# Kernel optimization log

Measured on AMD Instinct MI355X. Metric: run time of the kernel, lower is better.

Reference implementation:

```python
import jax, jax.numpy as jnp
import numpy as np

DT = 0.05      # bsde.delta_t
EPS = 1e-6     # BatchNormalization epsilon


def _bn(x, gamma, beta):
    # training-mode batch norm: statistics over the batch axis
    m = jnp.mean(x, axis=0, keepdims=True)
    v = jnp.var(x, axis=0, keepdims=True)
    return (x - m) * jax.lax.rsqrt(v + EPS) * gamma + beta


def _subnet(x, g0, b0, W0, g1, b1, W1, g2, b2, W2, bias2, g3, b3):
    # bn -> (dense -> bn -> relu) x 2 -> dense(+bias) -> bn
    x = _bn(x, g0, b0)
    x = jax.nn.relu(_bn(x @ W0, g1, b1))
    x = jax.nn.relu(_bn(x @ W1, g2, b2))
    x = _bn(x @ W2 + bias2, g3, b3)
    return x


def setup_inputs() -> dict:
    key = jax.random.key(0)
    B, D, N, H = 8192, 100, 20, 110
    T = N - 1  # number of subnets
    ks = jax.random.split(key, 18)
    u = lambda k, s, lo, hi: jax.random.uniform(k, s, jnp.float32, lo, hi)
    s_dh = np.sqrt(2.0 / (D + H)).astype(np.float32)
    s_hh = np.sqrt(2.0 / (H + H)).astype(np.float32)
    s_hd = np.sqrt(2.0 / (H + D)).astype(np.float32)
    return {
        "dw": jax.random.normal(ks[0], (B, D, N), jnp.float32) * np.sqrt(DT).astype(np.float32),
        "x": jax.random.normal(ks[1], (B, D, N + 1), jnp.float32),
        "mean_y_input": jax.random.normal(ks[2], (N,), jnp.float32),
        "y_init": u(ks[3], (1,), 0.0, 1.0),
        "z_init": u(ks[4], (1, D), -0.1, 0.1),
        "gamma0": u(ks[5], (T, D), 0.1, 0.5),
        "beta0": 0.1 * jax.random.normal(ks[6], (T, D), jnp.float32),
        "W0": s_dh * jax.random.normal(ks[7], (T, D, H), jnp.float32),
        "gamma1": u(ks[8], (T, H), 0.1, 0.5),
        "beta1": 0.1 * jax.random.normal(ks[9], (T, H), jnp.float32),
        "W1": s_hh * jax.random.normal(ks[10], (T, H, H), jnp.float32),
        "gamma2": u(ks[11], (T, H), 0.1, 0.5),
        "beta2": 0.1 * jax.random.normal(ks[12], (T, H), jnp.float32),
        "W2": s_hd * jax.random.normal(ks[13], (T, H, D), jnp.float32),
        "bias2": jnp.zeros((T, D), jnp.float32),
        "gamma3": u(ks[14], (T, D), 0.1, 0.5),
        "beta3": 0.1 * jax.random.normal(ks[15], (T, D), jnp.float32),
    }


def reference(dw, x, mean_y_input, y_init, z_init, gamma0, beta0, W0,
              gamma1, beta1, W1, gamma2, beta2, W2, bias2, gamma3, beta3):
    B, D, N = dw.shape
    T = N - 1
    # z at step t+1 depends only on x[:, :, t+1] and subnet t -> compute all in parallel
    x_steps = jnp.moveaxis(x[:, :, 1:N], 2, 0)  # [T, B, D]
    z_all = jax.vmap(_subnet)(x_steps, gamma0, beta0, W0, gamma1, beta1, W1,
                              gamma2, beta2, W2, bias2, gamma3, beta3) / D  # [T, B, D]
    z0 = jnp.broadcast_to(z_init, (B, D))          # all_one_vec @ z_init
    zs = jnp.concatenate([z0[None], z_all], axis=0)  # [N, B, D] (z used at each update)
    dw_steps = jnp.moveaxis(dw, 2, 0)               # [N, B, D]
    y0 = jnp.ones((B, 1), dw.dtype) * y_init

    def step(y, zd):
        z, dwt = zd
        # f_tf(t, x, y, z) = sin(y) for the SineBM equation
        y_new = y - DT * jnp.sin(y) + jnp.sum(z * dwt, axis=1, keepdims=True)
        return y_new, jnp.mean(y_new)

    y_final, means = jax.lax.scan(step, y0, (zs, dw_steps))
    mean_y = jnp.concatenate([jnp.mean(y0)[None], means[:T]])  # length N
    return y_final, mean_y
```

## Files before the change

### kernel.cpp

```cpp
#include <hip/hip_runtime.h>

typedef unsigned short u16;
typedef unsigned int   u32;

#define BATCH  8192
#define DIM    100
#define HID    110
#define TSUB   19
#define NSTEP  20
#define KP     128
#define NPAD   112
#define BN_EPS 1e-6f
#define DT_C   0.05f

#define SAB  1024
#define SAR  (BATCH / SAB)
#define SLICES 32

#define A3P  101

typedef __bf16 v8bf __attribute__((ext_vector_type(8)));
typedef float  v4f  __attribute__((ext_vector_type(4)));
typedef float  v2f  __attribute__((ext_vector_type(2)));
typedef u16    u16x4 __attribute__((ext_vector_type(4)));

__device__ __forceinline__ u16 f2bf(float f) {
    u32 u = __float_as_uint(f);
    return (u16)((u + 0x7fffu + ((u >> 16) & 1u)) >> 16);
}
__device__ __forceinline__ float bf2f(u16 h) {
    return __uint_as_float(((u32)h) << 16);
}
__device__ __forceinline__ void acc4(float4& s, float4& q, float4 v) {
    s.x += v.x; s.y += v.y; s.z += v.z; s.w += v.w;
    q.x += v.x * v.x; q.y += v.y * v.y; q.z += v.z * v.z; q.w += v.w * v.w;
}

__global__ void statsA(const float* __restrict__ x, float* __restrict__ part,
                       u32* __restrict__ xT32) {
    __shared__ u16 xls[SAR][2112];
    const int tid = threadIdx.x;
    const int b0 = blockIdx.x * SAR;
    float4 s0 = {0,0,0,0}, q0 = {0,0,0,0};
    float4 s1 = {0,0,0,0}, q1 = {0,0,0,0};
    float4 s2 = {0,0,0,0}, q2 = {0,0,0,0};
#pragma unroll
    for (int r = 0; r < SAR; r++) {
        const float4* row = (const float4*)(x + (size_t)(b0 + r) * 2100);
        float4 v0 = row[tid];
        float4 v1 = row[tid + 256];
        acc4(s0, q0, v0);
        acc4(s1, q1, v1);
        u16x4 p0 = { f2bf(v0.x), f2bf(v0.y), f2bf(v0.z), f2bf(v0.w) };
        u16x4 p1 = { f2bf(v1.x), f2bf(v1.y), f2bf(v1.z), f2bf(v1.w) };
        *(u16x4*)&xls[r][tid * 4]        = p0;
        *(u16x4*)&xls[r][1024 + tid * 4] = p1;
        if (tid < 13) {
            float4 v2 = row[tid + 512];
            acc4(s2, q2, v2);
            u16x4 p2 = { f2bf(v2.x), f2bf(v2.y), f2bf(v2.z), f2bf(v2.w) };
            *(u16x4*)&xls[r][2048 + tid * 4] = p2;
        }
    }
    float* ps = part + (size_t)blockIdx.x * 4200;
    *(float4*)&ps[tid * 4]               = s0;
    *(float4*)&ps[1024 + tid * 4]        = s1;
    *(float4*)&ps[2100 + tid * 4]        = q0;
    *(float4*)&ps[2100 + 1024 + tid * 4] = q1;
    if (tid < 13) {
        *(float4*)&ps[2048 + tid * 4]        = s2;
        *(float4*)&ps[2100 + 2048 + tid * 4] = q2;
    }
    __syncthreads();
    const int TOT = TSUB * SAR * (NPAD / 2);
    for (int i = tid; i < TOT; i += 256) {
        int w = i % (NPAD / 2);
        int seg = i / (NPAD / 2);
        int r = seg % SAR, t = seg / SAR;
        int d0 = w * 2;
        u32 v = 0;
        if (d0 < DIM) {
            u16 lo = xls[r][d0 * 21 + t + 1];
            u16 hi = (d0 + 1 < DIM) ? xls[r][(d0 + 1) * 21 + t + 1] : (u16)0;
            v = (u32)lo | ((u32)hi << 16);
        }
        xT32[((size_t)t * BATCH + b0 + r) * (NPAD / 2) + w] = v;
    }
}

__global__ void statsB(const float* __restrict__ part, float* __restrict__ out) {
    int gid = blockIdx.x * 256 + threadIdx.x;
    if (gid >= 4200 * SLICES) return;
    int slice = gid / 4200;
    int o = gid - slice * 4200;
    const float* p = part + (size_t)slice * (SAB / SLICES) * 4200 + o;
    float acc = 0.f;
#pragma unroll 4
    for (int i = 0; i < SAB / SLICES; i++) acc += p[(size_t)i * 4200];
    atomicAdd(&out[o], acc);
}

__global__ void wtrans(const float* __restrict__ W0, const float* __restrict__ W1,
                       const float* __restrict__ W2, u16* __restrict__ WTsw) {
    __shared__ float lw[HID * HID];
    const int t = blockIdx.x, l = blockIdx.y, tid = threadIdx.x;
    const float* W; int K, N;
    if (l == 0)      { W = W0; K = DIM; N = HID; }
    else if (l == 1) { W = W1; K = HID; N = HID; }
    else             { W = W2; K = HID; N = DIM; }
    const float* Wt = W + (size_t)t * K * N;
    for (int i = tid; i < K * N; i += 256) lw[i] = Wt[i];
    __syncthreads();
    u16* out = WTsw + ((size_t)l * TSUB + t) * (NPAD * KP);
    for (int i = tid; i < NPAD * 16; i += 256) {
        int n = i / 16, p = i % 16;
        int kc = p ^ (n & 7);
        u16 o8[8];
#pragma unroll
        for (int j = 0; j < 8; j++) {
            int k = kc * 8 + j;
            float v = (k < K && n < N) ? lw[k * N + n] : 0.f;
            o8[j] = f2bf(v);
        }
        *(uint4*)&out[(size_t)n * KP + p * 8] = *(uint4*)o8;
    }
}

template <int KREAL, int NOUT, int IDXMODE, int RELU, int BMAJOR>
__global__ void gemm_kernel(const u16* __restrict__ Ain,
                            const u16* __restrict__ WTswL,
                            const float* __restrict__ sumIn,
                            const float* __restrict__ sqIn,
                            const float* __restrict__ gIn,
                            const float* __restrict__ bIn,
                            u16* __restrict__ Hout,
                            float* __restrict__ sumArr,
                            float* __restrict__ sqArr) {
    __shared__ __align__(16) u16 Alds[128 * KP];
    __shared__ __align__(16) u16 Blds[NPAD * KP];
    __shared__ float s_sum[NPAD], s_sq[NPAD];
    __shared__ float aAffL[KP], cAffL[KP];

    const int tid = threadIdx.x;
    const int mt = blockIdx.x;
    const int t  = blockIdx.y;
    const int brow0 = mt * 128;

    if (tid < NPAD) { s_sum[tid] = 0.f; s_sq[tid] = 0.f; }
    if (tid < KREAL) {
        int idx = (IDXMODE == 0) ? (tid * 21 + (t + 1)) : (t * KREAL + tid);
        float m = sumIn[idx] * (1.f / BATCH);
        float v = sqIn[idx] * (1.f / BATCH) - m * m;
        float rstd = rsqrtf(v + BN_EPS);
        float ga = gIn[t * KREAL + tid] * rstd;
        aAffL[tid] = ga;
        cAffL[tid] = bIn[t * KREAL + tid] - m * ga;
    }

    {
        const uint4* wsrc = (const uint4*)(WTswL + (size_t)t * NPAD * KP);
        uint4* bl = (uint4*)Blds;
#pragma unroll
        for (int i = 0; i < 7; i++) bl[tid + i * 256] = wsrc[tid + i * 256];
    }
    const int NCH = (KREAL + 7) / 8;
    for (int i = tid; i < 128 * (16 - NCH); i += 256) {
        int row = i / (16 - NCH);
        int kc  = NCH + i % (16 - NCH);
        uint4 z = {0, 0, 0, 0};
        *(uint4*)&Alds[row * KP + (kc ^ (row & 7)) * 8] = z;
    }
    __syncthreads();

    for (int cidx = tid; cidx < 128 * NCH; cidx += 256) {
        int row = cidx / NCH;
        int kc  = cidx % NCH;
        int k0  = kc * 8;
        const u16* hrow = Ain + ((size_t)t * BATCH + brow0 + row) * NPAD + k0;
        u16 hv[8];
        *(uint4*)hv = *(const uint4*)hrow;
        u16 pk[8];
#pragma unroll
        for (int j = 0; j < 8; j++) {
            int k = k0 + j;
            float av = (k < KREAL) ? fmaf(bf2f(hv[j]), aAffL[k], cAffL[k]) : 0.f;
            if (RELU) av = fmaxf(av, 0.f);
            pk[j] = f2bf(av);
        }
        *(uint4*)&Alds[row * KP + ((kc ^ (row & 7)) * 8)] = *(uint4*)pk;
    }
    __syncthreads();

    const int lane = tid & 63;
    const int wv   = tid >> 6;
    const int r0   = lane & 15;
    const int q    = lane >> 4;
    const int moff = wv * 32;

    v4f acc[2][7];
#pragma unroll
    for (int i = 0; i < 2; i++)
#pragma unroll
        for (int j = 0; j < 7; j++) { v4f z = {0.f, 0.f, 0.f, 0.f}; acc[i][j] = z; }

#pragma unroll
    for (int ks = 0; ks < 4; ks++) {
        int cbase = ks * 4 + q;
        v8bf afr[2];
#pragma unroll
        for (int mf = 0; mf < 2; mf++) {
            int row = moff + mf * 16 + r0;
            afr[mf] = *(const v8bf*)&Alds[row * KP + ((cbase ^ (row & 7)) * 8)];
        }
#pragma unroll
        for (int nf = 0; nf < 7; nf++) {
            int nr = nf * 16 + r0;
            v8bf bfr = *(const v8bf*)&Blds[nr * KP + ((cbase ^ (nr & 7)) * 8)];
            acc[0][nf] = __builtin_amdgcn_mfma_f32_16x16x32_bf16(afr[0], bfr, acc[0][nf], 0, 0, 0);
            acc[1][nf] = __builtin_amdgcn_mfma_f32_16x16x32_bf16(afr[1], bfr, acc[1][nf], 0, 0, 0);
        }
    }

#pragma unroll
    for (int mf = 0; mf < 2; mf++) {
#pragma unroll
        for (int nf = 0; nf < 7; nf++) {
            int n = nf * 16 + r0;
#pragma unroll
            for (int rg = 0; rg < 4; rg++) {
                int grow = brow0 + moff + mf * 16 + q * 4 + rg;
                size_t oidx = BMAJOR ? ((size_t)grow * (TSUB * NPAD) + (size_t)t * NPAD + n)
                                     : (((size_t)t * BATCH + grow) * NPAD + n);
                Hout[oidx] = f2bf(acc[mf][nf][rg]);
            }
        }
    }
#pragma unroll
    for (int nf = 0; nf < 7; nf++) {
        float cs = 0.f, cq = 0.f;
#pragma unroll
        for (int mf = 0; mf < 2; mf++)
#pragma unroll
            for (int rg = 0; rg < 4; rg++) {
                float vv = acc[mf][nf][rg];
                cs += vv; cq += vv * vv;
            }
        cs += __shfl_xor(cs, 16); cs += __shfl_xor(cs, 32);
        cq += __shfl_xor(cq, 16); cq += __shfl_xor(cq, 32);
        if (q == 0) {
            atomicAdd(&s_sum[nf * 16 + r0], cs);
            atomicAdd(&s_sq[nf * 16 + r0], cq);
        }
    }
    __syncthreads();
    if (tid < NOUT) {
        atomicAdd(&sumArr[t * NOUT + tid], s_sum[tid]);
        atomicAdd(&sqArr[t * NOUT + tid], s_sq[tid]);
    }
}

__global__ __launch_bounds__(256, 3)
void scan_kernel(const float* __restrict__ dw,
                 const u16* __restrict__ zbuf,
                 const float* __restrict__ sum3, const float* __restrict__ sq3,
                 const float* __restrict__ g3, const float* __restrict__ b3,
                 const float* __restrict__ z_init, const float* __restrict__ y_init,
                 float* __restrict__ yout, float* __restrict__ meanout) {
    __shared__ float a3l[TSUB * A3P], c3l[TSUB * A3P];
    __shared__ float bsum[NSTEP];
    const int tid = threadIdx.x;
    for (int i = tid; i < TSUB * DIM; i += 256) {
        int t = i / DIM, d = i - t * DIM;
        float m = sum3[i] * (1.f / BATCH);
        float v = sq3[i] * (1.f / BATCH) - m * m;
        float rstd = rsqrtf(v + BN_EPS);
        float ga = g3[i] * rstd;
        a3l[t * A3P + d] = ga * (1.f / DIM);
        c3l[t * A3P + d] = (b3[i] - m * ga) * (1.f / DIM);
    }
    if (tid < NSTEP) bsum[tid] = 0.f;
    __syncthreads();

    const int wv = tid >> 6, lane = tid & 63;
    const int b = blockIdx.x * 4 + wv;
    const int ll = (lane < 50) ? lane : 49;

    v4f w[10];
    u32 zr[TSUB];
    v2f zi;
    {
        const float* dwaddr = dw + (size_t)b * (DIM * NSTEP) + ll * 40;
        const u16*   zaddr  = zbuf + (size_t)b * (TSUB * NPAD) + 2 * ll;
        const float* ziaddr = z_init + 2 * ll;
        asm volatile("global_load_dwordx4 %0, %1, off offset:0"   : "=v"(w[0]) : "v"(dwaddr));
        asm volatile("global_load_dwordx4 %0, %1, off offset:16"  : "=v"(w[1]) : "v"(dwaddr));
        asm volatile("global_load_dwordx4 %0, %1, off offset:32"  : "=v"(w[2]) : "v"(dwaddr));
        asm volatile("global_load_dwordx4 %0, %1, off offset:48"  : "=v"(w[3]) : "v"(dwaddr));
        asm volatile("global_load_dwordx4 %0, %1, off offset:64"  : "=v"(w[4]) : "v"(dwaddr));
        asm volatile("global_load_dwordx4 %0, %1, off offset:80"  : "=v"(w[5]) : "v"(dwaddr));
        asm volatile("global_load_dwordx4 %0, %1, off offset:96"  : "=v"(w[6]) : "v"(dwaddr));
        asm volatile("global_load_dwordx4 %0, %1, off offset:112" : "=v"(w[7]) : "v"(dwaddr));
        asm volatile("global_load_dwordx4 %0, %1, off offset:128" : "=v"(w[8]) : "v"(dwaddr));
        asm volatile("global_load_dwordx4 %0, %1, off offset:144" : "=v"(w[9]) : "v"(dwaddr));
#pragma unroll
        for (int t = 0; t < TSUB; t++)
            asm volatile("global_load_dword %0, %1, off offset:%2"
                         : "=v"(zr[t]) : "v"(zaddr), "i"(t * NPAD * 2));
        asm volatile("global_load_dwordx2 %0, %1, off" : "=v"(zi) : "v"(ziaddr));
        asm volatile("s_waitcnt vmcnt(0)" ::: "memory");
        __builtin_amdgcn_sched_barrier(0);
    }

    float acc[NSTEP];
#pragma unroll
    for (int k = 0; k < NSTEP; k++) acc[k] = 0.f;
    if (lane < 50) {
        const int dbase = 2 * lane;
        acc[0] = zi[0] * w[0][0] + zi[1] * w[5][0];
#pragma unroll
        for (int t = 0; t < TSUB; t++) {
            float a0 = a3l[t * A3P + dbase],     c0 = c3l[t * A3P + dbase];
            float a1 = a3l[t * A3P + dbase + 1], c1 = c3l[t * A3P + dbase + 1];
            u32 z = zr[t];
            float za0 = fmaf(bf2f((u16)(z & 0xffffu)), a0, c0);
            float za1 = fmaf(bf2f((u16)(z >> 16)),     a1, c1);
            const int n = t + 1, j = n >> 2, k = n & 3;
            acc[n] += w[j][k] * za0 + w[5 + j][k] * za1;
        }
    }

#pragma unroll
    for (int m = 1; m < 64; m <<= 1) {
#pragma unroll
        for (int k = 0; k < NSTEP; k++) acc[k] += __shfl_xor(acc[k], m, 64);
    }

    const float yi = y_init[0];
    float y = yi, ysave = 0.f;
#pragma unroll
    for (int i = 0; i < NSTEP; i++) {
        y = y - DT_C * __sinf(y) + acc[i];
        if (i == lane - 1) ysave = y;
    }
    if (lane == 0) yout[b] = y;
    if (lane >= 1 && lane < NSTEP) atomicAdd(&bsum[lane], ysave);
    __syncthreads();
    if (tid >= 1 && tid < NSTEP) atomicAdd(&meanout[tid], bsum[tid] * (1.f / BATCH));
    if (blockIdx.x == 0 && tid == 0) meanout[0] = yi;
}

extern "C" void kernel_launch(void* const* d_in, const int* in_sizes, int n_in,
                              void* d_out, int out_size, void* d_ws, size_t ws_size,
                              hipStream_t stream) {
    const float* dw     = (const float*)d_in[0];
    const float* x      = (const float*)d_in[1];
    const float* y_init = (const float*)d_in[3];
    const float* z_init = (const float*)d_in[4];
    const float* g0 = (const float*)d_in[5];
    const float* b0 = (const float*)d_in[6];
    const float* W0 = (const float*)d_in[7];
    const float* g1 = (const float*)d_in[8];
    const float* b1 = (const float*)d_in[9];
    const float* W1 = (const float*)d_in[10];
    const float* g2 = (const float*)d_in[11];
    const float* b2 = (const float*)d_in[12];
    const float* W2 = (const float*)d_in[13];
    const float* g3 = (const float*)d_in[15];
    const float* b3 = (const float*)d_in[16];

    char* ws = (char*)d_ws;
    size_t off = 0;
    auto alloc = [&](size_t bytes) -> void* {
        off = (off + 255) & ~(size_t)255;
        void* p = ws + off;
        off += bytes;
        return p;
    };

    const int nStats = 4200 + TSUB * HID * 2 * 2 + TSUB * DIM * 2;
    float* statsBlk = (float*)alloc((size_t)nStats * 4);
    float* sum0 = statsBlk;            float* sq0  = sum0 + 2100;
    float* sum1 = sum0 + 4200;         float* sq1  = sum1 + TSUB * HID;
    float* sum2 = sq1 + TSUB * HID;    float* sq2  = sum2 + TSUB * HID;
    float* sum3 = sq2 + TSUB * HID;    float* sq3  = sum3 + TSUB * DIM;

    u16* WTsw = (u16*)alloc((size_t)3 * TSUB * NPAD * KP * 2);

    const size_t hBytes = (size_t)TSUB * BATCH * NPAD * 2;
    u16* h0 = (u16*)alloc(hBytes);
    u16* h1 = (u16*)alloc(hBytes);
    u16* outbuf = h0;
    float* part = (float*)h0;
    u32*  xT32  = (u32*)h1;

    float* yout = (float*)d_out;
    float* meanout = yout + BATCH;

    hipMemsetAsync(statsBlk, 0, (size_t)nStats * 4, stream);
    hipMemsetAsync(meanout, 0, NSTEP * 4, stream);

    wtrans<<<dim3(TSUB, 3), 256, 0, stream>>>(W0, W1, W2, WTsw);
    statsA<<<SAB, 256, 0, stream>>>(x, part, xT32);
    statsB<<<(4200 * SLICES + 255) / 256, 256, 0, stream>>>(part, sum0);

    const u16* xT = (const u16*)xT32;
    u16* WT0 = WTsw;
    u16* WT1 = WTsw + (size_t)TSUB * NPAD * KP;
    u16* WT2 = WTsw + (size_t)2 * TSUB * NPAD * KP;

    gemm_kernel<DIM, HID, 0, 0, 0><<<dim3(64, TSUB), 256, 0, stream>>>(xT, WT0, sum0, sq0, g0, b0, h0, sum1, sq1);
    gemm_kernel<HID, HID, 1, 1, 0><<<dim3(64, TSUB), 256, 0, stream>>>(h0, WT1, sum1, sq1, g1, b1, h1, sum2, sq2);
    gemm_kernel<HID, DIM, 1, 1, 1><<<dim3(64, TSUB), 256, 0, stream>>>(h1, WT2, sum2, sq2, g2, b2, outbuf, sum3, sq3);

    scan_kernel<<<2048, 256, 0, stream>>>(dw, outbuf, sum3, sq3, g3, b3, z_init, y_init, yout, meanout);
}
```

Baseline: 195.6 us.

## Precompute final BN coefficients in separate kernel and stage scan inputs via coalesced LDS loads

Moves the per-block recomputation of the last batch-norm scale and shift (done by all 2048 scan blocks) into a tiny finalize3 kernel that writes packed float4 coefficients once. The scan kernel now loads each block's dw and z rows cooperatively with coalesced float4/u32 loads into swizzled shared memory instead of per-lane strided global loads. This cuts redundant rsqrt work and uncoalesced traffic, but adds an extra kernel launch and a block-wide barrier before compute.

```diff
diff --git a/kernel.cpp b/kernel.cpp
--- a/kernel.cpp
+++ b/kernel.cpp
@@ -17,11 +17,8 @@
 #define SAR  (BATCH / SAB)
 #define SLICES 32
 
-#define A3P  101
-
 typedef __bf16 v8bf __attribute__((ext_vector_type(8)));
 typedef float  v4f  __attribute__((ext_vector_type(4)));
-typedef float  v2f  __attribute__((ext_vector_type(2)));
 typedef u16    u16x4 __attribute__((ext_vector_type(4)));
 
 __device__ __forceinline__ u16 f2bf(float f) {
@@ -259,71 +256,75 @@
     }
 }
 
+__global__ void finalize3(const float* __restrict__ sum3, const float* __restrict__ sq3,
+                          const float* __restrict__ g3, const float* __restrict__ b3,
+                          float4* __restrict__ acg) {
+    int i = blockIdx.x * 256 + threadIdx.x;
+    if (i >= TSUB * 50) return;
+    int t = i / 50, p = i - t * 50;
+    int e = t * DIM + 2 * p;
+    float4 o;
+#pragma unroll
+    for (int h = 0; h < 2; h++) {
+        float m = sum3[e + h] * (1.f / BATCH);
+        float v = sq3[e + h] * (1.f / BATCH) - m * m;
+        float rstd = rsqrtf(v + BN_EPS);
+        float ga = g3[e + h] * rstd * (1.f / DIM);
+        float cc = b3[e + h] * (1.f / DIM) - m * ga;
+        if (h == 0) { o.x = ga; o.y = cc; } else { o.z = ga; o.w = cc; }
+    }
+    acg[i] = o;
+}
+
 __global__ __launch_bounds__(256, 3)
 void scan_kernel(const float* __restrict__ dw,
                  const u16* __restrict__ zbuf,
-                 const float* __restrict__ sum3, const float* __restrict__ sq3,
-                 const float* __restrict__ g3, const float* __restrict__ b3,
+                 const float4* __restrict__ acg,
                  const float* __restrict__ z_init, const float* __restrict__ y_init,
                  float* __restrict__ yout, float* __restrict__ meanout) {
-    __shared__ float a3l[TSUB * A3P], c3l[TSUB * A3P];
+    __shared__ __align__(16) float dwlds[4 * 512 * 4];
+    __shared__ u32 zlds[4 * 1064];
     __shared__ float bsum[NSTEP];
     const int tid = threadIdx.x;
-    for (int i = tid; i < TSUB * DIM; i += 256) {
-        int t = i / DIM, d = i - t * DIM;
-        float m = sum3[i] * (1.f / BATCH);
-        float v = sq3[i] * (1.f / BATCH) - m * m;
-        float rstd = rsqrtf(v + BN_EPS);
-        float ga = g3[i] * rstd;
-        a3l[t * A3P + d] = ga * (1.f / DIM);
-        c3l[t * A3P + d] = (b3[i] - m * ga) * (1.f / DIM);
-    }
+    const int b0 = blockIdx.x * 4;
+
+    const float4* dwg = (const float4*)(dw + (size_t)b0 * (DIM * NSTEP));
+    for (int c = tid; c < 2000; c += 256) {
+        int row = c / 500, cr = c - row * 500;
+        int sw = cr ^ ((cr >> 3) & 7);
+        *(float4*)&dwlds[(row * 512 + sw) * 4] = dwg[c];
+    }
+    const u32* zg = (const u32*)(zbuf + (size_t)b0 * (TSUB * NPAD));
+    for (int u = tid; u < 4 * 1064; u += 256) zlds[u] = zg[u];
     if (tid < NSTEP) bsum[tid] = 0.f;
     __syncthreads();
 
     const int wv = tid >> 6, lane = tid & 63;
-    const int b = blockIdx.x * 4 + wv;
+    const int b = b0 + wv;
     const int ll = (lane < 50) ? lane : 49;
 
     v4f w[10];
-    u32 zr[TSUB];
-    v2f zi;
-    {
-        const float* dwaddr = dw + (size_t)b * (DIM * NSTEP) + ll * 40;
-        const u16*   zaddr  = zbuf + (size_t)b * (TSUB * NPAD) + 2 * ll;
-        const float* ziaddr = z_init + 2 * ll;
-        asm volatile("global_load_dwordx4 %0, %1, off offset:0"   : "=v"(w[0]) : "v"(dwaddr));
-        asm volatile("global_load_dwordx4 %0, %1, off offset:16"  : "=v"(w[1]) : "v"(dwaddr));
-        asm volatile("global_load_dwordx4 %0, %1, off offset:32"  : "=v"(w[2]) : "v"(dwaddr));
-        asm volatile("global_load_dwordx4 %0, %1, off offset:48"  : "=v"(w[3]) : "v"(dwaddr));
-        asm volatile("global_load_dwordx4 %0, %1, off offset:64"  : "=v"(w[4]) : "v"(dwaddr));
-        asm volatile("global_load_dwordx4 %0, %1, off offset:80"  : "=v"(w[5]) : "v"(dwaddr));
-        asm volatile("global_load_dwordx4 %0, %1, off offset:96"  : "=v"(w[6]) : "v"(dwaddr));
-        asm volatile("global_load_dwordx4 %0, %1, off offset:112" : "=v"(w[7]) : "v"(dwaddr));
-        asm volatile("global_load_dwordx4 %0, %1, off offset:128" : "=v"(w[8]) : "v"(dwaddr));
-        asm volatile("global_load_dwordx4 %0, %1, off offset:144" : "=v"(w[9]) : "v"(dwaddr));
-#pragma unroll
-        for (int t = 0; t < TSUB; t++)
-            asm volatile("global_load_dword %0, %1, off offset:%2"
-                         : "=v"(zr[t]) : "v"(zaddr), "i"(t * NPAD * 2));
-        asm volatile("global_load_dwordx2 %0, %1, off" : "=v"(zi) : "v"(ziaddr));
-        asm volatile("s_waitcnt vmcnt(0)" ::: "memory");
-        __builtin_amdgcn_sched_barrier(0);
+    const float* dwbase = &dwlds[wv * 512 * 4];
+#pragma unroll
+    for (int j = 0; j < 10; j++) {
+        int cr = ll * 10 + j;
+        int sw = cr ^ ((cr >> 3) & 7);
+        w[j] = *(const v4f*)&dwbase[sw * 4];
     }
 
     float acc[NSTEP];
 #pragma unroll
     for (int k = 0; k < NSTEP; k++) acc[k] = 0.f;
     if (lane < 50) {
-        const int dbase = 2 * lane;
-        acc[0] = zi[0] * w[0][0] + zi[1] * w[5][0];
+        float2 zi = *(const float2*)(z_init + 2 * ll);
+        acc[0] = zi.x * w[0][0] + zi.y * w[5][0];
+        const u32* zrow = &zlds[wv * 1064];
 #pragma unroll
         for (int t = 0; t < TSUB; t++) {
-            float a0 = a3l[t * A3P + dbase],     c0 = c3l[t * A3P + dbase];
-            float a1 = a3l[t * A3P + dbase + 1], c1 = c3l[t * A3P + dbase + 1];
-            u32 z = zr[t];
-            float za0 = fmaf(bf2f((u16)(z & 0xffffu)), a0, c0);
-            float za1 = fmaf(bf2f((u16)(z >> 16)),     a1, c1);
+            float4 ac = acg[t * 50 + ll];
+            u32 z = zrow[t * 56 + ll];
+            float za0 = fmaf(bf2f((u16)(z & 0xffffu)), ac.x, ac.y);
+            float za1 = fmaf(bf2f((u16)(z >> 16)),     ac.z, ac.w);
             const int n = t + 1, j = n >> 2, k = n & 3;
             acc[n] += w[j][k] * za0 + w[5 + j][k] * za1;
         }
@@ -385,6 +386,7 @@
     float* sum3 = sq2 + TSUB * HID;    float* sq3  = sum3 + TSUB * DIM;
 
     u16* WTsw = (u16*)alloc((size_t)3 * TSUB * NPAD * KP * 2);
+    float4* acg = (float4*)alloc((size_t)TSUB * 50 * 16);
 
     const size_t hBytes = (size_t)TSUB * BATCH * NPAD * 2;
     u16* h0 = (u16*)alloc(hBytes);
@@ -412,5 +414,6 @@
     gemm_kernel<HID, HID, 1, 1, 0><<<dim3(64, TSUB), 256, 0, stream>>>(h0, WT1, sum1, sq1, g1, b1, h1, sum2, sq2);
     gemm_kernel<HID, DIM, 1, 1, 1><<<dim3(64, TSUB), 256, 0, stream>>>(h1, WT2, sum2, sq2, g2, b2, outbuf, sum3, sq3);
 
-    scan_kernel<<<2048, 256, 0, stream>>>(dw, outbuf, sum3, sq3, g3, b3, z_init, y_init, yout, meanout);
-}
+    finalize3<<<4, 256, 0, stream>>>(sum3, sq3, g3, b3, acg);
+    scan_kernel<<<2048, 256, 0, stream>>>(dw, outbuf, acg, z_init, y_init, yout, meanout);
+}
```

New measurement: 202.9 us. +3.7%, slower.

## Widen GEMM blocks to 512 threads, hoist BN3 finalize, replace mean atomics

Applied to the files above, without the earlier changes.

The three GEMM kernels now launch 512 threads per block, with each wave owning 16 rows instead of 32. This halves per-thread accumulators and adds more waves to hide latency, while LDS usage per block stays the same. The BN3 affine coefficients are computed once in a small finalize kernel instead of in every scan block, removing redundant per-block prologue work and 15KB of shared memory. The global atomic mean accumulation is replaced by per-block partials plus a separate reduction kernel, which costs two extra launches.

```diff
diff --git a/kernel.cpp b/kernel.cpp
--- a/kernel.cpp
+++ b/kernel.cpp
@@ -16,8 +16,7 @@
 #define SAB  1024
 #define SAR  (BATCH / SAB)
 #define SLICES 32
-
-#define A3P  101
+#define NBLK_SCAN 2048
 
 typedef __bf16 v8bf __attribute__((ext_vector_type(8)));
 typedef float  v4f  __attribute__((ext_vector_type(4)));
@@ -127,15 +126,16 @@
 }
 
 template <int KREAL, int NOUT, int IDXMODE, int RELU, int BMAJOR>
-__global__ void gemm_kernel(const u16* __restrict__ Ain,
-                            const u16* __restrict__ WTswL,
-                            const float* __restrict__ sumIn,
-                            const float* __restrict__ sqIn,
-                            const float* __restrict__ gIn,
-                            const float* __restrict__ bIn,
-                            u16* __restrict__ Hout,
-                            float* __restrict__ sumArr,
-                            float* __restrict__ sqArr) {
+__global__ __launch_bounds__(512, 2)
+void gemm_kernel(const u16* __restrict__ Ain,
+                 const u16* __restrict__ WTswL,
+                 const float* __restrict__ sumIn,
+                 const float* __restrict__ sqIn,
+                 const float* __restrict__ gIn,
+                 const float* __restrict__ bIn,
+                 u16* __restrict__ Hout,
+                 float* __restrict__ sumArr,
+                 float* __restrict__ sqArr) {
     __shared__ __align__(16) u16 Alds[128 * KP];
     __shared__ __align__(16) u16 Blds[NPAD * KP];
     __shared__ float s_sum[NPAD], s_sq[NPAD];
@@ -160,11 +160,10 @@
     {
         const uint4* wsrc = (const uint4*)(WTswL + (size_t)t * NPAD * KP);
         uint4* bl = (uint4*)Blds;
-#pragma unroll
-        for (int i = 0; i < 7; i++) bl[tid + i * 256] = wsrc[tid + i * 256];
+        for (int i = tid; i < NPAD * KP / 8; i += 512) bl[i] = wsrc[i];
     }
     const int NCH = (KREAL + 7) / 8;
-    for (int i = tid; i < 128 * (16 - NCH); i += 256) {
+    for (int i = tid; i < 128 * (16 - NCH); i += 512) {
         int row = i / (16 - NCH);
         int kc  = NCH + i % (16 - NCH);
         uint4 z = {0, 0, 0, 0};
@@ -172,7 +171,7 @@
     }
     __syncthreads();
 
-    for (int cidx = tid; cidx < 128 * NCH; cidx += 256) {
+    for (int cidx = tid; cidx < 128 * NCH; cidx += 512) {
         int row = cidx / NCH;
         int kc  = cidx % NCH;
         int k0  = kc * 8;
@@ -195,56 +194,44 @@
     const int wv   = tid >> 6;
     const int r0   = lane & 15;
     const int q    = lane >> 4;
-    const int moff = wv * 32;
-
-    v4f acc[2][7];
-#pragma unroll
-    for (int i = 0; i < 2; i++)
-#pragma unroll
-        for (int j = 0; j < 7; j++) { v4f z = {0.f, 0.f, 0.f, 0.f}; acc[i][j] = z; }
+    const int moff = wv * 16;
+
+    v4f acc[7];
+#pragma unroll
+    for (int j = 0; j < 7; j++) { v4f z = {0.f, 0.f, 0.f, 0.f}; acc[j] = z; }
 
 #pragma unroll
     for (int ks = 0; ks < 4; ks++) {
         int cbase = ks * 4 + q;
-        v8bf afr[2];
-#pragma unroll
-        for (int mf = 0; mf < 2; mf++) {
-            int row = moff + mf * 16 + r0;
-            afr[mf] = *(const v8bf*)&Alds[row * KP + ((cbase ^ (row & 7)) * 8)];
-        }
+        int row = moff + r0;
+        v8bf afr = *(const v8bf*)&Alds[row * KP + ((cbase ^ (row & 7)) * 8)];
 #pragma unroll
         for (int nf = 0; nf < 7; nf++) {
             int nr = nf * 16 + r0;
             v8bf bfr = *(const v8bf*)&Blds[nr * KP + ((cbase ^ (nr & 7)) * 8)];
-            acc[0][nf] = __builtin_amdgcn_mfma_f32_16x16x32_bf16(afr[0], bfr, acc[0][nf], 0, 0, 0);
-            acc[1][nf] = __builtin_amdgcn_mfma_f32_16x16x32_bf16(afr[1], bfr, acc[1][nf], 0, 0, 0);
-        }
-    }
-
-#pragma unroll
-    for (int mf = 0; mf < 2; mf++) {
-#pragma unroll
-        for (int nf = 0; nf < 7; nf++) {
-            int n = nf * 16 + r0;
-#pragma unroll
-            for (int rg = 0; rg < 4; rg++) {
-                int grow = brow0 + moff + mf * 16 + q * 4 + rg;
-                size_t oidx = BMAJOR ? ((size_t)grow * (TSUB * NPAD) + (size_t)t * NPAD + n)
-                                     : (((size_t)t * BATCH + grow) * NPAD + n);
-                Hout[oidx] = f2bf(acc[mf][nf][rg]);
-            }
+            acc[nf] = __builtin_amdgcn_mfma_f32_16x16x32_bf16(afr, bfr, acc[nf], 0, 0, 0);
+        }
+    }
+
+#pragma unroll
+    for (int nf = 0; nf < 7; nf++) {
+        int n = nf * 16 + r0;
+#pragma unroll
+        for (int rg = 0; rg < 4; rg++) {
+            int grow = brow0 + moff + q * 4 + rg;
+            size_t oidx = BMAJOR ? ((size_t)grow * (TSUB * NPAD) + (size_t)t * NPAD + n)
+                                 : (((size_t)t * BATCH + grow) * NPAD + n);
+            Hout[oidx] = f2bf(acc[nf][rg]);
         }
     }
 #pragma unroll
     for (int nf = 0; nf < 7; nf++) {
         float cs = 0.f, cq = 0.f;
 #pragma unroll
-        for (int mf = 0; mf < 2; mf++)
-#pragma unroll
-            for (int rg = 0; rg < 4; rg++) {
-                float vv = acc[mf][nf][rg];
-                cs += vv; cq += vv * vv;
-            }
+        for (int rg = 0; rg < 4; rg++) {
+            float vv = acc[nf][rg];
+            cs += vv; cq += vv * vv;
+        }
         cs += __shfl_xor(cs, 16); cs += __shfl_xor(cs, 32);
         cq += __shfl_xor(cq, 16); cq += __shfl_xor(cq, 32);
         if (q == 0) {
@@ -259,25 +246,34 @@
     }
 }
 
+__global__ void finalize3(const float* __restrict__ sum3, const float* __restrict__ sq3,
+                          const float* __restrict__ g3, const float* __restrict__ b3,
+                          float4* __restrict__ acg) {
+    int i = blockIdx.x * 256 + threadIdx.x;
+    if (i >= TSUB * 50) return;
+    int t = i / 50, p = i - t * 50;
+    int e = t * DIM + 2 * p;
+    float4 o;
+#pragma unroll
+    for (int h = 0; h < 2; h++) {
+        float m = sum3[e + h] * (1.f / BATCH);
+        float v = sq3[e + h] * (1.f / BATCH) - m * m;
+        float rstd = rsqrtf(v + BN_EPS);
+        float ga = g3[e + h] * rstd * (1.f / DIM);
+        float cc = b3[e + h] * (1.f / DIM) - m * ga;
+        if (h == 0) { o.x = ga; o.y = cc; } else { o.z = ga; o.w = cc; }
+    }
+    acg[i] = o;
+}
+
 __global__ __launch_bounds__(256, 3)
 void scan_kernel(const float* __restrict__ dw,
                  const u16* __restrict__ zbuf,
-                 const float* __restrict__ sum3, const float* __restrict__ sq3,
-                 const float* __restrict__ g3, const float* __restrict__ b3,
+                 const float4* __restrict__ acg,
                  const float* __restrict__ z_init, const float* __restrict__ y_init,
-                 float* __restrict__ yout, float* __restrict__ meanout) {
-    __shared__ float a3l[TSUB * A3P], c3l[TSUB * A3P];
+                 float* __restrict__ yout, float* __restrict__ mred) {
     __shared__ float bsum[NSTEP];
     const int tid = threadIdx.x;
-    for (int i = tid; i < TSUB * DIM; i += 256) {
-        int t = i / DIM, d = i - t * DIM;
-        float m = sum3[i] * (1.f / BATCH);
-        float v = sq3[i] * (1.f / BATCH) - m * m;
-        float rstd = rsqrtf(v + BN_EPS);
-        float ga = g3[i] * rstd;
-        a3l[t * A3P + d] = ga * (1.f / DIM);
-        c3l[t * A3P + d] = (b3[i] - m * ga) * (1.f / DIM);
-    }
     if (tid < NSTEP) bsum[tid] = 0.f;
     __syncthreads();
 
@@ -315,15 +311,13 @@
 #pragma unroll
     for (int k = 0; k < NSTEP; k++) acc[k] = 0.f;
     if (lane < 50) {
-        const int dbase = 2 * lane;
         acc[0] = zi[0] * w[0][0] + zi[1] * w[5][0];
 #pragma unroll
         for (int t = 0; t < TSUB; t++) {
-            float a0 = a3l[t * A3P + dbase],     c0 = c3l[t * A3P + dbase];
-            float a1 = a3l[t * A3P + dbase + 1], c1 = c3l[t * A3P + dbase + 1];
+            float4 ac = acg[t * 50 + ll];
             u32 z = zr[t];
-            float za0 = fmaf(bf2f((u16)(z & 0xffffu)), a0, c0);
-            float za1 = fmaf(bf2f((u16)(z >> 16)),     a1, c1);
+            float za0 = fmaf(bf2f((u16)(z & 0xffffu)), ac.x, ac.y);
+            float za1 = fmaf(bf2f((u16)(z >> 16)),     ac.z, ac.w);
             const int n = t + 1, j = n >> 2, k = n & 3;
             acc[n] += w[j][k] * za0 + w[5 + j][k] * za1;
         }
@@ -345,8 +339,21 @@
     if (lane == 0) yout[b] = y;
     if (lane >= 1 && lane < NSTEP) atomicAdd(&bsum[lane], ysave);
     __syncthreads();
-    if (tid >= 1 && tid < NSTEP) atomicAdd(&meanout[tid], bsum[tid] * (1.f / BATCH));
-    if (blockIdx.x == 0 && tid == 0) meanout[0] = yi;
+    if (tid >= 1 && tid < NSTEP) mred[blockIdx.x * NSTEP + tid] = bsum[tid];
+}
+
+__global__ void meanred(const float* __restrict__ mred, const float* __restrict__ y_init,
+                        float* __restrict__ meanout) {
+    const int n = blockIdx.x, tid = threadIdx.x;
+    if (n == 0) { if (tid == 0) meanout[0] = y_init[0]; return; }
+    float s = 0.f;
+    for (int i = tid; i < NBLK_SCAN; i += 256) s += mred[(size_t)i * NSTEP + n];
+#pragma unroll
+    for (int m = 1; m < 64; m <<= 1) s += __shfl_xor(s, m, 64);
+    __shared__ float ws4[4];
+    if ((tid & 63) == 0) ws4[tid >> 6] = s;
+    __syncthreads();
+    if (tid == 0) meanout[n] = (ws4[0] + ws4[1] + ws4[2] + ws4[3]) * (1.f / BATCH);
 }
 
 extern "C" void kernel_launch(void* const* d_in, const int* in_sizes, int n_in,
@@ -385,6 +392,8 @@
     float* sum3 = sq2 + TSUB * HID;    float* sq3  = sum3 + TSUB * DIM;
 
     u16* WTsw = (u16*)alloc((size_t)3 * TSUB * NPAD * KP * 2);
+    float4* acg = (float4*)alloc((size_t)TSUB * 50 * 16);
+    float* mred = (float*)alloc((size_t)NBLK_SCAN * NSTEP * 4);
 
     const size_t hBytes = (size_t)TSUB * BATCH * NPAD * 2;
     u16* h0 = (u16*)alloc(hBytes);
@@ -397,7 +406,6 @@
     float* meanout = yout + BATCH;
 
     hipMemsetAsync(statsBlk, 0, (size_t)nStats * 4, stream);
-    hipMemsetAsync(meanout, 0, NSTEP * 4, stream);
 
     wtrans<<<dim3(TSUB, 3), 256, 0, stream>>>(W0, W1, W2, WTsw);
     statsA<<<SAB, 256, 0, stream>>>(x, part, xT32);
@@ -408,9 +416,11 @@
     u16* WT1 = WTsw + (size_t)TSUB * NPAD * KP;
     u16* WT2 = WTsw + (size_t)2 * TSUB * NPAD * KP;
 
-    gemm_kernel<DIM, HID, 0, 0, 0><<<dim3(64, TSUB), 256, 0, stream>>>(xT, WT0, sum0, sq0, g0, b0, h0, sum1, sq1);
-    gemm_kernel<HID, HID, 1, 1, 0><<<dim3(64, TSUB), 256, 0, stream>>>(h0, WT1, sum1, sq1, g1, b1, h1, sum2, sq2);
-    gemm_kernel<HID, DIM, 1, 1, 1><<<dim3(64, TSUB), 256, 0, stream>>>(h1, WT2, sum2, sq2, g2, b2, outbuf, sum3, sq3);
-
-    scan_kernel<<<2048, 256, 0, stream>>>(dw, outbuf, sum3, sq3, g3, b3, z_init, y_init, yout, meanout);
-}
+    gemm_kernel<DIM, HID, 0, 0, 0><<<dim3(64, TSUB), 512, 0, stream>>>(xT, WT0, sum0, sq0, g0, b0, h0, sum1, sq1);
+    gemm_kernel<HID, HID, 1, 1, 0><<<dim3(64, TSUB), 512, 0, stream>>>(h0, WT1, sum1, sq1, g1, b1, h1, sum2, sq2);
+    gemm_kernel<HID, DIM, 1, 1, 1><<<dim3(64, TSUB), 512, 0, stream>>>(h1, WT2, sum2, sq2, g2, b2, outbuf, sum3, sq3);
+
+    finalize3<<<4, 256, 0, stream>>>(sum3, sq3, g3, b3, acg);
+    scan_kernel<<<NBLK_SCAN, 256, 0, stream>>>(dw, outbuf, acg, z_init, y_init, yout, mred);
+    meanred<<<NSTEP, 256, 0, stream>>>(mred, y_init, meanout);
+}
```

Result: faster. 182.2 us (-6.8%).
